# Optimization experiments

Hardware: AMD Instinct MI355X
Metric: run time of the kernel (lower is better)

The kernel has to match this reference:

```python
import jax, jax.numpy as jnp
import numpy as np

N = 50000
E = 800000
D_IN = 128
D_OUT = 128


def setup_inputs() -> dict:
    key = jax.random.key(0)
    ks = jax.random.split(key, 12)
    x = jax.random.normal(ks[0], (N, D_IN), dtype=jnp.float32)
    W1 = jax.random.normal(ks[1], (D_IN, D_OUT), dtype=jnp.float32) * (1.0 / np.sqrt(D_IN))
    b1 = jnp.zeros((D_OUT,), dtype=jnp.float32)
    W2 = jax.random.normal(ks[2], (D_IN, D_OUT), dtype=jnp.float32) * (1.0 / np.sqrt(D_IN))
    b2 = jnp.zeros((D_OUT,), dtype=jnp.float32)
    # inverted-dropout masks, p=0.5 -> values in {0, 2}
    def mask(k):
        return jnp.where(jax.random.uniform(k, (N, D_IN)) < 0.5, 0.0, 2.0).astype(jnp.float32)
    mask_pos1 = mask(ks[3])
    mask_neg1 = mask(ks[4])
    mask_pos2 = mask(ks[5])
    mask_neg2 = mask(ks[6])
    edge_index1 = jax.random.randint(ks[7], (2, E), 0, N, dtype=jnp.int32)
    edge_index2 = jax.random.randint(ks[8], (2, E), 0, N, dtype=jnp.int32)
    perm1 = jax.random.permutation(ks[9], N).astype(jnp.int32)
    perm2 = jax.random.permutation(ks[10], N).astype(jnp.int32)
    return dict(x=x, W1=W1, b1=b1, W2=W2, b2=b2,
                mask_pos1=mask_pos1, mask_neg1=mask_neg1,
                mask_pos2=mask_pos2, mask_neg2=mask_neg2,
                edge_index1=edge_index1, edge_index2=edge_index2,
                perm1=perm1, perm2=perm2)


def gcn_conv(x, W, b, edge_index):
    """PyG GCNConv: add self-loops, symmetric normalization, then x@W aggregation + bias."""
    n = x.shape[0]
    xw = x @ W  # [N, D_OUT]
    loops = jnp.arange(n, dtype=edge_index.dtype)
    src = jnp.concatenate([edge_index[0], loops])
    dst = jnp.concatenate([edge_index[1], loops])
    deg = jax.ops.segment_sum(jnp.ones_like(dst, dtype=xw.dtype), dst, num_segments=n)
    dinv = jax.lax.rsqrt(jnp.maximum(deg, 1.0))  # deg >= 1 due to self-loops
    norm = dinv[src] * dinv[dst]                 # [E+N]
    msg = xw[src] * norm[:, None]                # [E+N, D_OUT]
    out = jax.ops.segment_sum(msg, dst, num_segments=n)
    return out + b


def _branch(x, W, b, edge_index, mask_pos, mask_neg, perm):
    pos_h = jax.nn.relu(gcn_conv(x * mask_pos, W, b, edge_index))
    neg_in = (x * mask_neg)[perm]
    neg_h = jax.nn.relu(gcn_conv(neg_in, W, b, edge_index))
    summary = jnp.mean(pos_h, axis=0, keepdims=True)  # [1, D_OUT]
    return pos_h, neg_h, summary


def reference(x, W1, b1, W2, b2, mask_pos1, mask_neg1, mask_pos2, mask_neg2,
              edge_index1, edge_index2, perm1, perm2):
    p1, n1, s1 = _branch(x, W1, b1, edge_index1, mask_pos1, mask_neg1, perm1)
    p2, n2, s2 = _branch(x, W2, b2, edge_index2, mask_pos2, mask_neg2, perm2)
    return (p1, n1, s1, p2, n2, s2)
```

## Files before the change

kernel.cpp:

```cpp
#include <hip/hip_runtime.h>
#include <hip/hip_fp16.h>

#define NN 50000
#define NE 800000
#define D 128
#define GEMM_BLOCKS 3128
#define NBKT 64
#define BW 782
#define SCAP 2048

typedef _Float16 half8_t __attribute__((ext_vector_type(8)));
typedef _Float16 half4_t __attribute__((ext_vector_type(4)));
typedef float f32x4 __attribute__((ext_vector_type(4)));

__global__ void k_init(float* s1, float* s2, int* bcnt,
                       const float* __restrict__ W1, const float* __restrict__ W2,
                       _Float16* wt1, _Float16* wt2,
                       const int* __restrict__ perm1, const int* __restrict__ perm2,
                       int* pinv1, int* pinv2) {
    int i = blockIdx.x * 256 + threadIdx.x;
    if (i < NN) { pinv1[perm1[i]] = i; pinv2[perm2[i]] = i; }
    if (i < 1024) bcnt[i] = 0;
    if (i < D) { s1[i] = 0.f; s2[i] = 0.f; }
    if (i < 16384) {
        int n = i >> 7, k = i & 127;
        wt1[n * 128 + k] = (_Float16)W1[k * 128 + n];
        wt2[n * 128 + k] = (_Float16)W2[k * 128 + n];
    }
}

__global__ void k_bucket(const int* __restrict__ src1, const int* __restrict__ dst1,
                         const int* __restrict__ src2, const int* __restrict__ dst2,
                         int* bcnt, int2* bsd1, int2* bsd2) {
    __shared__ int lcnt[128], lpos[128], gbase[128];
    int t = threadIdx.x;
    int sl = blockIdx.x & 7;
    if (t < 128) { lcnt[t] = 0; lpos[t] = 0; }
    __syncthreads();

    int e0 = blockIdx.x * 256 + t;
    int s1v0=0,d1v0=0,s2v0=0,d2v0=0, s1v1=0,d1v1=0,s2v1=0,d2v1=0;
    int s1v2=0,d1v2=0,s2v2=0,d2v2=0, s1v3=0,d1v3=0,s2v3=0,d2v3=0;
    bool v0 = (e0 + 0 * 262144) < NE;
    bool v1 = (e0 + 1 * 262144) < NE;
    bool v2 = (e0 + 2 * 262144) < NE;
    bool v3 = (e0 + 3 * 262144) < NE;
    if (v0) { int e = e0;             s1v0 = src1[e]; d1v0 = dst1[e]; s2v0 = src2[e]; d2v0 = dst2[e]; }
    if (v1) { int e = e0 + 262144;    s1v1 = src1[e]; d1v1 = dst1[e]; s2v1 = src2[e]; d2v1 = dst2[e]; }
    if (v2) { int e = e0 + 2*262144;  s1v2 = src1[e]; d1v2 = dst1[e]; s2v2 = src2[e]; d2v2 = dst2[e]; }
    if (v3) { int e = e0 + 3*262144;  s1v3 = src1[e]; d1v3 = dst1[e]; s2v3 = src2[e]; d2v3 = dst2[e]; }

    if (v0) { atomicAdd(&lcnt[d1v0 / BW], 1); atomicAdd(&lcnt[NBKT + d2v0 / BW], 1); }
    if (v1) { atomicAdd(&lcnt[d1v1 / BW], 1); atomicAdd(&lcnt[NBKT + d2v1 / BW], 1); }
    if (v2) { atomicAdd(&lcnt[d1v2 / BW], 1); atomicAdd(&lcnt[NBKT + d2v2 / BW], 1); }
    if (v3) { atomicAdd(&lcnt[d1v3 / BW], 1); atomicAdd(&lcnt[NBKT + d2v3 / BW], 1); }
    __syncthreads();
    if (t < 128) gbase[t] = atomicAdd(&bcnt[t * 8 + sl], lcnt[t]);
    __syncthreads();

    #define PLACE(sv, dv) { \
        int r = (dv) / BW; \
        int p = gbase[r] + atomicAdd(&lpos[r], 1); \
        if (p < SCAP) bsd1[(r * 8 + sl) * SCAP + p] = make_int2((sv), (dv)); }
    #define PLACE2(sv, dv) { \
        int r = (dv) / BW; \
        int p = gbase[NBKT + r] + atomicAdd(&lpos[NBKT + r], 1); \
        if (p < SCAP) bsd2[(r * 8 + sl) * SCAP + p] = make_int2((sv), (dv)); }
    if (v0) { PLACE(s1v0, d1v0); PLACE2(s2v0, d2v0); }
    if (v1) { PLACE(s1v1, d1v1); PLACE2(s2v1, d2v1); }
    if (v2) { PLACE(s1v2, d1v2); PLACE2(s2v2, d2v2); }
    if (v3) { PLACE(s1v3, d1v3); PLACE2(s2v3, d2v3); }
    #undef PLACE
    #undef PLACE2
}

__launch_bounds__(512)
__global__ void k_build(const int* __restrict__ bcnt,
                        const int2* __restrict__ bsd1, const int2* __restrict__ bsd2,
                        int* rp1, int* rp2, int* col1, int* col2,
                        float* dinv1, float* dinv2) {
    __shared__ int h[1024];
    __shared__ int tsum[512];
    __shared__ int tb[64];
    __shared__ int ns[8];
    __shared__ int bbase;
    int t = threadIdx.x;
    int g = blockIdx.x >> 6;
    int f = blockIdx.x & 63;
    const int2* bsd = (g ? bsd2 : bsd1) + f * 8 * SCAP;
    int* rp = g ? rp2 : rp1;
    int* col = g ? col2 : col1;
    float* dinv = g ? dinv2 : dinv1;

    h[t] = 0; h[t + 512] = 0;
    if (t < 8) {
        int v = bcnt[(g * NBKT + f) * 8 + t];
        ns[t] = (v > SCAP) ? SCAP : v;
    }
    if (t < NBKT) {
        int tot = 0;
        #pragma unroll
        for (int s = 0; s < 8; s++) tot += bcnt[(g * NBKT + t) * 8 + s];
        tb[t] = tot;
    }
    __syncthreads();

    #pragma unroll
    for (int s = 0; s < 8; s++) {
        int n = ns[s];
        const int2* seg = bsd + s * SCAP;
        for (int i = t; i < n; i += 512) atomicAdd(&h[seg[i].y - f * BW], 1);
    }
    __syncthreads();
    if (t == 0) { int b = 0; for (int j = 0; j < f; j++) b += tb[j]; bbase = b; }

    int a0 = h[2 * t], a1 = h[2 * t + 1];
    int s = a0 + a1;
    tsum[t] = s;
    __syncthreads();
    for (int off = 1; off < 512; off <<= 1) {
        int add = (t >= off) ? tsum[t - off] : 0;
        __syncthreads();
        tsum[t] += add;
        __syncthreads();
    }
    int excl = tsum[t] - s + bbase;
    int idx = 2 * t, gd = f * BW + idx;
    int e0 = excl, e1 = excl + a0;
    h[2 * t] = e0; h[2 * t + 1] = e1;
    if (idx < BW && gd < NN)         { rp[gd]     = e0; dinv[gd]     = rsqrtf((float)(a0 + 1)); }
    if (idx + 1 < BW && gd + 1 < NN) { rp[gd + 1] = e1; dinv[gd + 1] = rsqrtf((float)(a1 + 1)); }
    if (f == 63 && t == 0) rp[NN] = NE;
    __syncthreads();

    #pragma unroll
    for (int sg = 0; sg < 8; sg++) {
        int n = ns[sg];
        const int2* seg = bsd + sg * SCAP;
        for (int i = t; i < n; i += 512) {
            int2 e = seg[i];
            int p = atomicAdd(&h[e.y - f * BW], 1);
            col[p] = e.x;
        }
    }
}

__launch_bounds__(256)
__global__ void k_gemm(const _Float16* __restrict__ wt1, const _Float16* __restrict__ wt2,
                       const float* __restrict__ x,
                       const float* __restrict__ mp1, const float* __restrict__ mn1,
                       const float* __restrict__ mp2, const float* __restrict__ mn2,
                       const int* __restrict__ pinv1, const int* __restrict__ pinv2,
                       const float* __restrict__ dinv1, const float* __restrict__ dinv2,
                       _Float16* xwi1, _Float16* xwi2) {
    __shared__ __align__(16) _Float16 ST[4][16][136];

    int g = blockIdx.x;
    int which = g / 782;
    int bx = g - which * 782;
    const _Float16* wt = (which < 2) ? wt1 : wt2;
    const float* mask = (which == 0) ? mp1 : (which == 1) ? mn1 : (which == 2) ? mp2 : mn2;
    const int* pinv = (which == 1) ? pinv1 : (which == 3) ? pinv2 : nullptr;
    const float* dinv = (which < 2) ? dinv1 : dinv2;
    _Float16* out = ((which < 2) ? xwi1 : xwi2) + ((which & 1) ? 128 : 0);

    int t = threadIdx.x;
    int wave = t >> 6;
    int lane = t & 63;
    int quad = lane >> 4;
    int m = lane & 15;
    int tile = bx * 4 + wave;
    if (tile * 16 >= NN) return;

    int row = tile * 16 + m;
    const float* xrow = x + (long)row * D;
    const float* mrow = mask + (long)row * D;

    half8_t a[4];
    #pragma unroll
    for (int kk = 0; kk < 4; kk++) {
        int k0 = kk * 32 + quad * 8;
        f32x4 xa = *(const f32x4*)(xrow + k0);
        f32x4 xb = *(const f32x4*)(xrow + k0 + 4);
        f32x4 ma = __builtin_nontemporal_load((const f32x4*)(mrow + k0));
        f32x4 mb = __builtin_nontemporal_load((const f32x4*)(mrow + k0 + 4));
        a[kk][0] = (_Float16)(xa[0] * ma[0]);
        a[kk][1] = (_Float16)(xa[1] * ma[1]);
        a[kk][2] = (_Float16)(xa[2] * ma[2]);
        a[kk][3] = (_Float16)(xa[3] * ma[3]);
        a[kk][4] = (_Float16)(xb[0] * mb[0]);
        a[kk][5] = (_Float16)(xb[1] * mb[1]);
        a[kk][6] = (_Float16)(xb[2] * mb[2]);
        a[kk][7] = (_Float16)(xb[3] * mb[3]);
    }

    f32x4 accs[8];
    #pragma unroll
    for (int nt = 0; nt < 8; nt++) {
        const _Float16* wrow = wt + (nt * 16 + m) * 128 + quad * 8;
        f32x4 acc = {0.f, 0.f, 0.f, 0.f};
        #pragma unroll
        for (int kk = 0; kk < 4; kk++) {
            half8_t w = *(const half8_t*)(wrow + kk * 32);
            acc = __builtin_amdgcn_mfma_f32_16x16x32_f16(w, a[kk], acc, 0, 0, 0);
        }
        accs[nt] = acc;
    }

    int orow = pinv ? pinv[row] : row;
    float ds = dinv[orow];
    _Float16* st = &ST[wave][0][0];

    #pragma unroll
    for (int nt = 0; nt < 8; nt++) {
        half4_t h;
        h[0] = (_Float16)(accs[nt][0] * ds);
        h[1] = (_Float16)(accs[nt][1] * ds);
        h[2] = (_Float16)(accs[nt][2] * ds);
        h[3] = (_Float16)(accs[nt][3] * ds);
        *(half4_t*)(st + m * 136 + nt * 16 + quad * 4) = h;
    }
    #pragma unroll
    for (int p = 0; p < 4; p++) {
        int cc = (lane >> 4) + p * 4;
        half8_t v = *(const half8_t*)(st + m * 136 + cc * 8);
        *(half8_t*)(out + (long)orow * 256 + cc * 8) = v;
    }
}

__launch_bounds__(256)
__global__ void k_agg(const _Float16* __restrict__ xwi1, const _Float16* __restrict__ xwi2,
                      const int* __restrict__ rp1, const int* __restrict__ col1,
                      const float* __restrict__ dinv1,
                      const int* __restrict__ rp2, const int* __restrict__ col2,
                      const float* __restrict__ dinv2,
                      const float* __restrict__ b1, const float* __restrict__ b2,
                      float* out) {
    int g = blockIdx.y;
    const _Float16* xwi = g ? xwi2 : xwi1;
    const int* rp = g ? rp2 : rp1;
    const int* col = g ? col2 : col1;
    const float* dinv = g ? dinv2 : dinv1;
    const float* bias = g ? b2 : b1;
    float* pos_out = out + (g ? 12800128L : 0L);
    float* neg_out = out + (g ? 19200128L : 6400000L);

    int t = threadIdx.x;
    int wave = t >> 6, lane = t & 63;
    int i = blockIdx.x * 4 + wave;
    if (i >= NN) return;
    int j4 = lane * 4;

    half4_t sv = *(const half4_t*)(xwi + (long)i * 256 + j4);
    float a0 = (float)sv[0], a1 = (float)sv[1], a2 = (float)sv[2], a3 = (float)sv[3];
    int e0 = rp[i], e1 = rp[i + 1];
    int e = e0;
    for (; e + 8 <= e1; e += 8) {
        int s0 = col[e + 0], s1 = col[e + 1], s2 = col[e + 2], s3 = col[e + 3];
        int s4 = col[e + 4], s5 = col[e + 5], s6 = col[e + 6], s7 = col[e + 7];
        half4_t v0 = *(const half4_t*)(xwi + (long)s0 * 256 + j4);
        half4_t v1 = *(const half4_t*)(xwi + (long)s1 * 256 + j4);
        half4_t v2 = *(const half4_t*)(xwi + (long)s2 * 256 + j4);
        half4_t v3 = *(const half4_t*)(xwi + (long)s3 * 256 + j4);
        half4_t v4 = *(const half4_t*)(xwi + (long)s4 * 256 + j4);
        half4_t v5 = *(const half4_t*)(xwi + (long)s5 * 256 + j4);
        half4_t v6 = *(const half4_t*)(xwi + (long)s6 * 256 + j4);
        half4_t v7 = *(const half4_t*)(xwi + (long)s7 * 256 + j4);
        a0 += (float)v0[0] + (float)v1[0] + (float)v2[0] + (float)v3[0]
            + (float)v4[0] + (float)v5[0] + (float)v6[0] + (float)v7[0];
        a1 += (float)v0[1] + (float)v1[1] + (float)v2[1] + (float)v3[1]
            + (float)v4[1] + (float)v5[1] + (float)v6[1] + (float)v7[1];
        a2 += (float)v0[2] + (float)v1[2] + (float)v2[2] + (float)v3[2]
            + (float)v4[2] + (float)v5[2] + (float)v6[2] + (float)v7[2];
        a3 += (float)v0[3] + (float)v1[3] + (float)v2[3] + (float)v3[3]
            + (float)v4[3] + (float)v5[3] + (float)v6[3] + (float)v7[3];
    }
    for (; e + 4 <= e1; e += 4) {
        int s0 = col[e + 0], s1 = col[e + 1], s2 = col[e + 2], s3 = col[e + 3];
        half4_t v0 = *(const half4_t*)(xwi + (long)s0 * 256 + j4);
        half4_t v1 = *(const half4_t*)(xwi + (long)s1 * 256 + j4);
        half4_t v2 = *(const half4_t*)(xwi + (long)s2 * 256 + j4);
        half4_t v3 = *(const half4_t*)(xwi + (long)s3 * 256 + j4);
        a0 += (float)v0[0] + (float)v1[0] + (float)v2[0] + (float)v3[0];
        a1 += (float)v0[1] + (float)v1[1] + (float)v2[1] + (float)v3[1];
        a2 += (float)v0[2] + (float)v1[2] + (float)v2[2] + (float)v3[2];
        a3 += (float)v0[3] + (float)v1[3] + (float)v2[3] + (float)v3[3];
    }
    for (; e < e1; e++) {
        int s = col[e];
        half4_t v = *(const half4_t*)(xwi + (long)s * 256 + j4);
        a0 += (float)v[0]; a1 += (float)v[1]; a2 += (float)v[2]; a3 += (float)v[3];
    }
    float di = dinv[i];
    int jj = (lane < 32) ? j4 : (j4 - 128);
    const f32x4* bp = (const f32x4*)(bias + jj);
    f32x4 bv = *bp;
    f32x4 o;
    o[0] = fmaxf(0.f, di * a0 + bv[0]);
    o[1] = fmaxf(0.f, di * a1 + bv[1]);
    o[2] = fmaxf(0.f, di * a2 + bv[2]);
    o[3] = fmaxf(0.f, di * a3 + bv[3]);
    float* dst = ((lane < 32) ? pos_out : neg_out) + (long)i * D + jj;
    __builtin_nontemporal_store(o, (f32x4*)dst);
}

__launch_bounds__(256)
__global__ void k_sum(const float* __restrict__ pos1, const float* __restrict__ pos2,
                      float* s1, float* s2) {
    int g = blockIdx.y;
    const float* pos = g ? pos2 : pos1;
    float* s = g ? s2 : s1;
    int t = threadIdx.x;
    int rg = t >> 5;
    int j = (t & 31) * 4;
    f32x4 acc = {0.f, 0.f, 0.f, 0.f};
    for (int i = blockIdx.x * 8 + rg; i < NN; i += gridDim.x * 8) {
        f32x4 v = __builtin_nontemporal_load((const f32x4*)(pos + (long)i * D + j));
        acc[0] += v[0]; acc[1] += v[1]; acc[2] += v[2]; acc[3] += v[3];
    }
    __shared__ float sm[8][128];
    sm[rg][j + 0] = acc[0];
    sm[rg][j + 1] = acc[1];
    sm[rg][j + 2] = acc[2];
    sm[rg][j + 3] = acc[3];
    __syncthreads();
    if (t < 128) {
        float v = 0.f;
        for (int r = 0; r < 8; r++) v += sm[r][t];
        atomicAdd(&s[t], v * (1.0f / NN));
    }
}

extern "C" void kernel_launch(void* const* d_in, const int* in_sizes, int n_in,
                              void* d_out, int out_size, void* d_ws, size_t ws_size,
                              hipStream_t stream) {
    const float* x   = (const float*)d_in[0];
    const float* W1  = (const float*)d_in[1];
    const float* b1  = (const float*)d_in[2];
    const float* W2  = (const float*)d_in[3];
    const float* b2  = (const float*)d_in[4];
    const float* mp1 = (const float*)d_in[5];
    const float* mn1 = (const float*)d_in[6];
    const float* mp2 = (const float*)d_in[7];
    const float* mn2 = (const float*)d_in[8];
    const int* e1 = (const int*)d_in[9];
    const int* e2 = (const int*)d_in[10];
    const int* perm1 = (const int*)d_in[11];
    const int* perm2 = (const int*)d_in[12];
    const int* src1 = e1;       const int* dst1 = e1 + NE;
    const int* src2 = e2;       const int* dst2 = e2 + NE;
    float* out = (float*)d_out;

    char* w = (char*)d_ws;
    _Float16* xwi1 = (_Float16*)w; w += (size_t)NN * 256 * 2;
    _Float16* xwi2 = (_Float16*)w; w += (size_t)NN * 256 * 2;
    int* rp1 = (int*)w;   w += (size_t)(NN + 4) * 4;
    int* rp2 = (int*)w;   w += (size_t)(NN + 4) * 4;
    int* col1 = (int*)w;  w += (size_t)NE * 4;
    int* col2 = (int*)w;  w += (size_t)NE * 4;
    float* dinv1 = (float*)w; w += (size_t)NN * 4;
    float* dinv2 = (float*)w; w += (size_t)NN * 4;
    int* bcnt  = (int*)w; w += (size_t)1024 * 4;
    int2* bsd1 = (int2*)w; w += (size_t)NBKT * 8 * SCAP * 8;
    int2* bsd2 = (int2*)w; w += (size_t)NBKT * 8 * SCAP * 8;
    _Float16* wt1 = (_Float16*)w; w += (size_t)D * D * 2;
    _Float16* wt2 = (_Float16*)w; w += (size_t)D * D * 2;
    int* pinv1 = (int*)w; w += (size_t)NN * 4;
    int* pinv2 = (int*)w; w += (size_t)NN * 4;

    float* s1 = out + 12800000L;
    float* s2 = out + 25600128L;
    const float* pos1 = out;
    const float* pos2 = out + 12800128L;

    k_init<<<dim3(196), 256, 0, stream>>>(s1, s2, bcnt, W1, W2, wt1, wt2,
                                          perm1, perm2, pinv1, pinv2);
    k_bucket<<<dim3(1024), 256, 0, stream>>>(src1, dst1, src2, dst2, bcnt, bsd1, bsd2);
    k_build<<<dim3(128), 512, 0, stream>>>(bcnt, bsd1, bsd2,
                                           rp1, rp2, col1, col2, dinv1, dinv2);
    k_gemm<<<dim3(GEMM_BLOCKS), 256, 0, stream>>>(wt1, wt2,
        x, mp1, mn1, mp2, mn2, pinv1, pinv2, dinv1, dinv2, xwi1, xwi2);
    k_agg<<<dim3(12500, 2), 256, 0, stream>>>(xwi1, xwi2,
                                              rp1, col1, dinv1, rp2, col2, dinv2,
                                              b1, b2, out);
    k_sum<<<dim3(512, 2), 256, 0, stream>>>(pos1, pos2, s1, s2);
}
```

Measured before the change: 455.4 us.

## Fuse edge bucketing with GEMM and move source-degree scaling into aggregation

The GEMM no longer depends on dinv, so it is merged into the same launch as edge bucketing as a horizontal fusion. Bucketing blocks and GEMM blocks can then run concurrently, and one kernel launch and a serial dependency on k_build are removed. To make this possible, the per-source dinv scaling moves from the GEMM epilogue into k_agg, which now gathers dinv[src] per edge. That adds extra scattered loads and multiplies in the aggregation loop.

```diff
diff --git a/kernel.cpp b/kernel.cpp
--- a/kernel.cpp
+++ b/kernel.cpp
@@ -4,6 +4,7 @@
 #define NN 50000
 #define NE 800000
 #define D 128
+#define BKT_BLOCKS 1024
 #define GEMM_BLOCKS 3128
 #define NBKT 64
 #define BW 782
@@ -29,49 +30,131 @@
     }
 }
 
-__global__ void k_bucket(const int* __restrict__ src1, const int* __restrict__ dst1,
-                         const int* __restrict__ src2, const int* __restrict__ dst2,
-                         int* bcnt, int2* bsd1, int2* bsd2) {
+__launch_bounds__(256)
+__global__ void k_bucket_gemm(const int* __restrict__ src1, const int* __restrict__ dst1,
+                              const int* __restrict__ src2, const int* __restrict__ dst2,
+                              int* bcnt, int2* bsd1, int2* bsd2,
+                              const _Float16* __restrict__ wt1, const _Float16* __restrict__ wt2,
+                              const float* __restrict__ x,
+                              const float* __restrict__ mp1, const float* __restrict__ mn1,
+                              const float* __restrict__ mp2, const float* __restrict__ mn2,
+                              const int* __restrict__ pinv1, const int* __restrict__ pinv2,
+                              _Float16* xwi1, _Float16* xwi2) {
     __shared__ int lcnt[128], lpos[128], gbase[128];
+    __shared__ __align__(16) _Float16 ST[4][16][136];
     int t = threadIdx.x;
-    int sl = blockIdx.x & 7;
-    if (t < 128) { lcnt[t] = 0; lpos[t] = 0; }
-    __syncthreads();
-
-    int e0 = blockIdx.x * 256 + t;
-    int s1v0=0,d1v0=0,s2v0=0,d2v0=0, s1v1=0,d1v1=0,s2v1=0,d2v1=0;
-    int s1v2=0,d1v2=0,s2v2=0,d2v2=0, s1v3=0,d1v3=0,s2v3=0,d2v3=0;
-    bool v0 = (e0 + 0 * 262144) < NE;
-    bool v1 = (e0 + 1 * 262144) < NE;
-    bool v2 = (e0 + 2 * 262144) < NE;
-    bool v3 = (e0 + 3 * 262144) < NE;
-    if (v0) { int e = e0;             s1v0 = src1[e]; d1v0 = dst1[e]; s2v0 = src2[e]; d2v0 = dst2[e]; }
-    if (v1) { int e = e0 + 262144;    s1v1 = src1[e]; d1v1 = dst1[e]; s2v1 = src2[e]; d2v1 = dst2[e]; }
-    if (v2) { int e = e0 + 2*262144;  s1v2 = src1[e]; d1v2 = dst1[e]; s2v2 = src2[e]; d2v2 = dst2[e]; }
-    if (v3) { int e = e0 + 3*262144;  s1v3 = src1[e]; d1v3 = dst1[e]; s2v3 = src2[e]; d2v3 = dst2[e]; }
-
-    if (v0) { atomicAdd(&lcnt[d1v0 / BW], 1); atomicAdd(&lcnt[NBKT + d2v0 / BW], 1); }
-    if (v1) { atomicAdd(&lcnt[d1v1 / BW], 1); atomicAdd(&lcnt[NBKT + d2v1 / BW], 1); }
-    if (v2) { atomicAdd(&lcnt[d1v2 / BW], 1); atomicAdd(&lcnt[NBKT + d2v2 / BW], 1); }
-    if (v3) { atomicAdd(&lcnt[d1v3 / BW], 1); atomicAdd(&lcnt[NBKT + d2v3 / BW], 1); }
-    __syncthreads();
-    if (t < 128) gbase[t] = atomicAdd(&bcnt[t * 8 + sl], lcnt[t]);
-    __syncthreads();
-
-    #define PLACE(sv, dv) { \
-        int r = (dv) / BW; \
-        int p = gbase[r] + atomicAdd(&lpos[r], 1); \
-        if (p < SCAP) bsd1[(r * 8 + sl) * SCAP + p] = make_int2((sv), (dv)); }
-    #define PLACE2(sv, dv) { \
-        int r = (dv) / BW; \
-        int p = gbase[NBKT + r] + atomicAdd(&lpos[NBKT + r], 1); \
-        if (p < SCAP) bsd2[(r * 8 + sl) * SCAP + p] = make_int2((sv), (dv)); }
-    if (v0) { PLACE(s1v0, d1v0); PLACE2(s2v0, d2v0); }
-    if (v1) { PLACE(s1v1, d1v1); PLACE2(s2v1, d2v1); }
-    if (v2) { PLACE(s1v2, d1v2); PLACE2(s2v2, d2v2); }
-    if (v3) { PLACE(s1v3, d1v3); PLACE2(s2v3, d2v3); }
-    #undef PLACE
-    #undef PLACE2
+    int bid = blockIdx.x;
+
+    if (bid < BKT_BLOCKS) {
+        int sl = bid & 7;
+        if (t < 128) { lcnt[t] = 0; lpos[t] = 0; }
+        __syncthreads();
+
+        int e0 = bid * 256 + t;
+        int s1v0=0,d1v0=0,s2v0=0,d2v0=0, s1v1=0,d1v1=0,s2v1=0,d2v1=0;
+        int s1v2=0,d1v2=0,s2v2=0,d2v2=0, s1v3=0,d1v3=0,s2v3=0,d2v3=0;
+        bool v0 = (e0 + 0 * 262144) < NE;
+        bool v1 = (e0 + 1 * 262144) < NE;
+        bool v2 = (e0 + 2 * 262144) < NE;
+        bool v3 = (e0 + 3 * 262144) < NE;
+        if (v0) { int e = e0;             s1v0 = src1[e]; d1v0 = dst1[e]; s2v0 = src2[e]; d2v0 = dst2[e]; }
+        if (v1) { int e = e0 + 262144;    s1v1 = src1[e]; d1v1 = dst1[e]; s2v1 = src2[e]; d2v1 = dst2[e]; }
+        if (v2) { int e = e0 + 2*262144;  s1v2 = src1[e]; d1v2 = dst1[e]; s2v2 = src2[e]; d2v2 = dst2[e]; }
+        if (v3) { int e = e0 + 3*262144;  s1v3 = src1[e]; d1v3 = dst1[e]; s2v3 = src2[e]; d2v3 = dst2[e]; }
+
+        if (v0) { atomicAdd(&lcnt[d1v0 / BW], 1); atomicAdd(&lcnt[NBKT + d2v0 / BW], 1); }
+        if (v1) { atomicAdd(&lcnt[d1v1 / BW], 1); atomicAdd(&lcnt[NBKT + d2v1 / BW], 1); }
+        if (v2) { atomicAdd(&lcnt[d1v2 / BW], 1); atomicAdd(&lcnt[NBKT + d2v2 / BW], 1); }
+        if (v3) { atomicAdd(&lcnt[d1v3 / BW], 1); atomicAdd(&lcnt[NBKT + d2v3 / BW], 1); }
+        __syncthreads();
+        if (t < 128) gbase[t] = atomicAdd(&bcnt[t * 8 + sl], lcnt[t]);
+        __syncthreads();
+
+        #define PLACE(sv, dv) { \
+            int r = (dv) / BW; \
+            int p = gbase[r] + atomicAdd(&lpos[r], 1); \
+            if (p < SCAP) bsd1[(r * 8 + sl) * SCAP + p] = make_int2((sv), (dv)); }
+        #define PLACE2(sv, dv) { \
+            int r = (dv) / BW; \
+            int p = gbase[NBKT + r] + atomicAdd(&lpos[NBKT + r], 1); \
+            if (p < SCAP) bsd2[(r * 8 + sl) * SCAP + p] = make_int2((sv), (dv)); }
+        if (v0) { PLACE(s1v0, d1v0); PLACE2(s2v0, d2v0); }
+        if (v1) { PLACE(s1v1, d1v1); PLACE2(s2v1, d2v1); }
+        if (v2) { PLACE(s1v2, d1v2); PLACE2(s2v2, d2v2); }
+        if (v3) { PLACE(s1v3, d1v3); PLACE2(s2v3, d2v3); }
+        #undef PLACE
+        #undef PLACE2
+        return;
+    }
+
+    int g = bid - BKT_BLOCKS;
+    int which = g / 782;
+    int bx = g - which * 782;
+    const _Float16* wt = (which < 2) ? wt1 : wt2;
+    const float* mask = (which == 0) ? mp1 : (which == 1) ? mn1 : (which == 2) ? mp2 : mn2;
+    const int* pinv = (which == 1) ? pinv1 : (which == 3) ? pinv2 : nullptr;
+    _Float16* out = ((which < 2) ? xwi1 : xwi2) + ((which & 1) ? 128 : 0);
+
+    int wave = t >> 6;
+    int lane = t & 63;
+    int quad = lane >> 4;
+    int m = lane & 15;
+    int tile = bx * 4 + wave;
+    if (tile * 16 >= NN) return;
+
+    int row = tile * 16 + m;
+    const float* xrow = x + (long)row * D;
+    const float* mrow = mask + (long)row * D;
+
+    half8_t a[4];
+    #pragma unroll
+    for (int kk = 0; kk < 4; kk++) {
+        int k0 = kk * 32 + quad * 8;
+        f32x4 xa = *(const f32x4*)(xrow + k0);
+        f32x4 xb = *(const f32x4*)(xrow + k0 + 4);
+        f32x4 ma = __builtin_nontemporal_load((const f32x4*)(mrow + k0));
+        f32x4 mb = __builtin_nontemporal_load((const f32x4*)(mrow + k0 + 4));
+        a[kk][0] = (_Float16)(xa[0] * ma[0]);
+        a[kk][1] = (_Float16)(xa[1] * ma[1]);
+        a[kk][2] = (_Float16)(xa[2] * ma[2]);
+        a[kk][3] = (_Float16)(xa[3] * ma[3]);
+        a[kk][4] = (_Float16)(xb[0] * mb[0]);
+        a[kk][5] = (_Float16)(xb[1] * mb[1]);
+        a[kk][6] = (_Float16)(xb[2] * mb[2]);
+        a[kk][7] = (_Float16)(xb[3] * mb[3]);
+    }
+
+    f32x4 accs[8];
+    #pragma unroll
+    for (int nt = 0; nt < 8; nt++) {
+        const _Float16* wrow = wt + (nt * 16 + m) * 128 + quad * 8;
+        f32x4 acc = {0.f, 0.f, 0.f, 0.f};
+        #pragma unroll
+        for (int kk = 0; kk < 4; kk++) {
+            half8_t w = *(const half8_t*)(wrow + kk * 32);
+            acc = __builtin_amdgcn_mfma_f32_16x16x32_f16(w, a[kk], acc, 0, 0, 0);
+        }
+        accs[nt] = acc;
+    }
+
+    int orow = pinv ? pinv[row] : row;
+    _Float16* st = &ST[wave][0][0];
+
+    #pragma unroll
+    for (int nt = 0; nt < 8; nt++) {
+        half4_t h;
+        h[0] = (_Float16)accs[nt][0];
+        h[1] = (_Float16)accs[nt][1];
+        h[2] = (_Float16)accs[nt][2];
+        h[3] = (_Float16)accs[nt][3];
+        *(half4_t*)(st + m * 136 + nt * 16 + quad * 4) = h;
+    }
+    #pragma unroll
+    for (int p = 0; p < 4; p++) {
+        int cc = (lane >> 4) + p * 4;
+        half8_t v = *(const half8_t*)(st + m * 136 + cc * 8);
+        *(half8_t*)(out + (long)orow * 256 + cc * 8) = v;
+    }
 }
 
 __launch_bounds__(512)
@@ -146,89 +229,6 @@
 }
 
 __launch_bounds__(256)
-__global__ void k_gemm(const _Float16* __restrict__ wt1, const _Float16* __restrict__ wt2,
-                       const float* __restrict__ x,
-                       const float* __restrict__ mp1, const float* __restrict__ mn1,
-                       const float* __restrict__ mp2, const float* __restrict__ mn2,
-                       const int* __restrict__ pinv1, const int* __restrict__ pinv2,
-                       const float* __restrict__ dinv1, const float* __restrict__ dinv2,
-                       _Float16* xwi1, _Float16* xwi2) {
-    __shared__ __align__(16) _Float16 ST[4][16][136];
-
-    int g = blockIdx.x;
-    int which = g / 782;
-    int bx = g - which * 782;
-    const _Float16* wt = (which < 2) ? wt1 : wt2;
-    const float* mask = (which == 0) ? mp1 : (which == 1) ? mn1 : (which == 2) ? mp2 : mn2;
-    const int* pinv = (which == 1) ? pinv1 : (which == 3) ? pinv2 : nullptr;
-    const float* dinv = (which < 2) ? dinv1 : dinv2;
-    _Float16* out = ((which < 2) ? xwi1 : xwi2) + ((which & 1) ? 128 : 0);
-
-    int t = threadIdx.x;
-    int wave = t >> 6;
-    int lane = t & 63;
-    int quad = lane >> 4;
-    int m = lane & 15;
-    int tile = bx * 4 + wave;
-    if (tile * 16 >= NN) return;
-
-    int row = tile * 16 + m;
-    const float* xrow = x + (long)row * D;
-    const float* mrow = mask + (long)row * D;
-
-    half8_t a[4];
-    #pragma unroll
-    for (int kk = 0; kk < 4; kk++) {
-        int k0 = kk * 32 + quad * 8;
-        f32x4 xa = *(const f32x4*)(xrow + k0);
-        f32x4 xb = *(const f32x4*)(xrow + k0 + 4);
-        f32x4 ma = __builtin_nontemporal_load((const f32x4*)(mrow + k0));
-        f32x4 mb = __builtin_nontemporal_load((const f32x4*)(mrow + k0 + 4));
-        a[kk][0] = (_Float16)(xa[0] * ma[0]);
-        a[kk][1] = (_Float16)(xa[1] * ma[1]);
-        a[kk][2] = (_Float16)(xa[2] * ma[2]);
-        a[kk][3] = (_Float16)(xa[3] * ma[3]);
-        a[kk][4] = (_Float16)(xb[0] * mb[0]);
-        a[kk][5] = (_Float16)(xb[1] * mb[1]);
-        a[kk][6] = (_Float16)(xb[2] * mb[2]);
-        a[kk][7] = (_Float16)(xb[3] * mb[3]);
-    }
-
-    f32x4 accs[8];
-    #pragma unroll
-    for (int nt = 0; nt < 8; nt++) {
-        const _Float16* wrow = wt + (nt * 16 + m) * 128 + quad * 8;
-        f32x4 acc = {0.f, 0.f, 0.f, 0.f};
-        #pragma unroll
-        for (int kk = 0; kk < 4; kk++) {
-            half8_t w = *(const half8_t*)(wrow + kk * 32);
-            acc = __builtin_amdgcn_mfma_f32_16x16x32_f16(w, a[kk], acc, 0, 0, 0);
-        }
-        accs[nt] = acc;
-    }
-
-    int orow = pinv ? pinv[row] : row;
-    float ds = dinv[orow];
-    _Float16* st = &ST[wave][0][0];
-
-    #pragma unroll
-    for (int nt = 0; nt < 8; nt++) {
-        half4_t h;
-        h[0] = (_Float16)(accs[nt][0] * ds);
-        h[1] = (_Float16)(accs[nt][1] * ds);
-        h[2] = (_Float16)(accs[nt][2] * ds);
-        h[3] = (_Float16)(accs[nt][3] * ds);
-        *(half4_t*)(st + m * 136 + nt * 16 + quad * 4) = h;
-    }
-    #pragma unroll
-    for (int p = 0; p < 4; p++) {
-        int cc = (lane >> 4) + p * 4;
-        half8_t v = *(const half8_t*)(st + m * 136 + cc * 8);
-        *(half8_t*)(out + (long)orow * 256 + cc * 8) = v;
-    }
-}
-
-__launch_bounds__(256)
 __global__ void k_agg(const _Float16* __restrict__ xwi1, const _Float16* __restrict__ xwi2,
                       const int* __restrict__ rp1, const int* __restrict__ col1,
                       const float* __restrict__ dinv1,
@@ -251,13 +251,17 @@
     if (i >= NN) return;
     int j4 = lane * 4;
 
+    float di = dinv[i];
     half4_t sv = *(const half4_t*)(xwi + (long)i * 256 + j4);
-    float a0 = (float)sv[0], a1 = (float)sv[1], a2 = (float)sv[2], a3 = (float)sv[3];
+    float a0 = di * (float)sv[0], a1 = di * (float)sv[1];
+    float a2 = di * (float)sv[2], a3 = di * (float)sv[3];
     int e0 = rp[i], e1 = rp[i + 1];
     int e = e0;
     for (; e + 8 <= e1; e += 8) {
         int s0 = col[e + 0], s1 = col[e + 1], s2 = col[e + 2], s3 = col[e + 3];
         int s4 = col[e + 4], s5 = col[e + 5], s6 = col[e + 6], s7 = col[e + 7];
+        float ds0 = dinv[s0], ds1 = dinv[s1], ds2 = dinv[s2], ds3 = dinv[s3];
+        float ds4 = dinv[s4], ds5 = dinv[s5], ds6 = dinv[s6], ds7 = dinv[s7];
         half4_t v0 = *(const half4_t*)(xwi + (long)s0 * 256 + j4);
         half4_t v1 = *(const half4_t*)(xwi + (long)s1 * 256 + j4);
         half4_t v2 = *(const half4_t*)(xwi + (long)s2 * 256 + j4);
@@ -266,32 +270,33 @@
         half4_t v5 = *(const half4_t*)(xwi + (long)s5 * 256 + j4);
         half4_t v6 = *(const half4_t*)(xwi + (long)s6 * 256 + j4);
         half4_t v7 = *(const half4_t*)(xwi + (long)s7 * 256 + j4);
-        a0 += (float)v0[0] + (float)v1[0] + (float)v2[0] + (float)v3[0]
-            + (float)v4[0] + (float)v5[0] + (float)v6[0] + (float)v7[0];
-        a1 += (float)v0[1] + (float)v1[1] + (float)v2[1] + (float)v3[1]
-            + (float)v4[1] + (float)v5[1] + (float)v6[1] + (float)v7[1];
-        a2 += (float)v0[2] + (float)v1[2] + (float)v2[2] + (float)v3[2]
-            + (float)v4[2] + (float)v5[2] + (float)v6[2] + (float)v7[2];
-        a3 += (float)v0[3] + (float)v1[3] + (float)v2[3] + (float)v3[3]
-            + (float)v4[3] + (float)v5[3] + (float)v6[3] + (float)v7[3];
+        a0 += ds0*(float)v0[0] + ds1*(float)v1[0] + ds2*(float)v2[0] + ds3*(float)v3[0]
+            + ds4*(float)v4[0] + ds5*(float)v5[0] + ds6*(float)v6[0] + ds7*(float)v7[0];
+        a1 += ds0*(float)v0[1] + ds1*(float)v1[1] + ds2*(float)v2[1] + ds3*(float)v3[1]
+            + ds4*(float)v4[1] + ds5*(float)v5[1] + ds6*(float)v6[1] + ds7*(float)v7[1];
+        a2 += ds0*(float)v0[2] + ds1*(float)v1[2] + ds2*(float)v2[2] + ds3*(float)v3[2]
+            + ds4*(float)v4[2] + ds5*(float)v5[2] + ds6*(float)v6[2] + ds7*(float)v7[2];
+        a3 += ds0*(float)v0[3] + ds1*(float)v1[3] + ds2*(float)v2[3] + ds3*(float)v3[3]
+            + ds4*(float)v4[3] + ds5*(float)v5[3] + ds6*(float)v6[3] + ds7*(float)v7[3];
     }
     for (; e + 4 <= e1; e += 4) {
         int s0 = col[e + 0], s1 = col[e + 1], s2 = col[e + 2], s3 = col[e + 3];
+        float ds0 = dinv[s0], ds1 = dinv[s1], ds2 = dinv[s2], ds3 = dinv[s3];
         half4_t v0 = *(const half4_t*)(xwi + (long)s0 * 256 + j4);
         half4_t v1 = *(const half4_t*)(xwi + (long)s1 * 256 + j4);
         half4_t v2 = *(const half4_t*)(xwi + (long)s2 * 256 + j4);
         half4_t v3 = *(const half4_t*)(xwi + (long)s3 * 256 + j4);
-        a0 += (float)v0[0] + (float)v1[0] + (float)v2[0] + (float)v3[0];
-        a1 += (float)v0[1] + (float)v1[1] + (float)v2[1] + (float)v3[1];
-        a2 += (float)v0[2] + (float)v1[2] + (float)v2[2] + (float)v3[2];
-        a3 += (float)v0[3] + (float)v1[3] + (float)v2[3] + (float)v3[3];
+        a0 += ds0*(float)v0[0] + ds1*(float)v1[0] + ds2*(float)v2[0] + ds3*(float)v3[0];
+        a1 += ds0*(float)v0[1] + ds1*(float)v1[1] + ds2*(float)v2[1] + ds3*(float)v3[1];
+        a2 += ds0*(float)v0[2] + ds1*(float)v1[2] + ds2*(float)v2[2] + ds3*(float)v3[2];
+        a3 += ds0*(float)v0[3] + ds1*(float)v1[3] + ds2*(float)v2[3] + ds3*(float)v3[3];
     }
     for (; e < e1; e++) {
         int s = col[e];
+        float ds = dinv[s];
         half4_t v = *(const half4_t*)(xwi + (long)s * 256 + j4);
-        a0 += (float)v[0]; a1 += (float)v[1]; a2 += (float)v[2]; a3 += (float)v[3];
-    }
-    float di = dinv[i];
+        a0 += ds*(float)v[0]; a1 += ds*(float)v[1]; a2 += ds*(float)v[2]; a3 += ds*(float)v[3];
+    }
     int jj = (lane < 32) ? j4 : (j4 - 128);
     const f32x4* bp = (const f32x4*)(bias + jj);
     f32x4 bv = *bp;
@@ -375,11 +380,11 @@
 
     k_init<<<dim3(196), 256, 0, stream>>>(s1, s2, bcnt, W1, W2, wt1, wt2,
                                           perm1, perm2, pinv1, pinv2);
-    k_bucket<<<dim3(1024), 256, 0, stream>>>(src1, dst1, src2, dst2, bcnt, bsd1, bsd2);
+    k_bucket_gemm<<<dim3(BKT_BLOCKS + GEMM_BLOCKS), 256, 0, stream>>>(
+        src1, dst1, src2, dst2, bcnt, bsd1, bsd2,
+        wt1, wt2, x, mp1, mn1, mp2, mn2, pinv1, pinv2, xwi1, xwi2);
     k_build<<<dim3(128), 512, 0, stream>>>(bcnt, bsd1, bsd2,
                                            rp1, rp2, col1, col2, dinv1, dinv2);
-    k_gemm<<<dim3(GEMM_BLOCKS), 256, 0, stream>>>(wt1, wt2,
-        x, mp1, mn1, mp2, mn2, pinv1, pinv2, dinv1, dinv2, xwi1, xwi2);
     k_agg<<<dim3(12500, 2), 256, 0, stream>>>(xwi1, xwi2,
                                               rp1, col1, dinv1, rp2, col2, dinv2,
                                               b1, b2, out);
```

Result: no change. 454.7 us (-0.2%).
